# Optimization experiments

Hardware: AMD Instinct MI355X
Metric: run time of the kernel (lower is better)

## Reference

```python
import jax, jax.numpy as jnp
import numpy as np

D_MODEL = 1024
N_HEADS = 16
D_K = 64
BATCH = 2
SEQ = 2048
LN_EPS = 1e-5


def setup_inputs() -> dict:
    key = jax.random.key(0)
    ks = jax.random.split(key, 6)
    s = 1.0 / np.sqrt(D_MODEL)
    return {
        "h": jax.random.normal(ks[0], (BATCH, SEQ, D_MODEL), dtype=jnp.float32),
        "Wq": jax.random.normal(ks[1], (D_MODEL, D_MODEL), dtype=jnp.float32) * s,
        "bq": jnp.zeros((D_MODEL,), jnp.float32),
        "Wk": jax.random.normal(ks[2], (D_MODEL, D_MODEL), dtype=jnp.float32) * s,
        "bk": jnp.zeros((D_MODEL,), jnp.float32),
        "Wv": jax.random.normal(ks[3], (D_MODEL, D_MODEL), dtype=jnp.float32) * s,
        "bv": jnp.zeros((D_MODEL,), jnp.float32),
        "Wo": jax.random.normal(ks[4], (D_MODEL, D_MODEL), dtype=jnp.float32) * s,
        "bo": jnp.zeros((D_MODEL,), jnp.float32),
        "ln_w": jnp.ones((D_MODEL,), jnp.float32),
        "ln_b": jnp.zeros((D_MODEL,), jnp.float32),
    }


def _layernorm(x, w, b):
    mu = jnp.mean(x, axis=-1, keepdims=True)
    var = jnp.var(x, axis=-1, keepdims=True)
    return (x - mu) * jax.lax.rsqrt(var + LN_EPS) * w + b


def reference(h, Wq, bq, Wk, bk, Wv, bv, Wo, bo, ln_w, ln_b):
    b, s, _ = h.shape
    scale = 1.0 / np.sqrt(D_K)
    h_res = h
    hn = _layernorm(h, ln_w, ln_b)
    # Linear layers (torch convention: y = x @ W.T + b), split into heads
    q = (hn @ Wq.T + bq).reshape(b, s, N_HEADS, D_K)
    k = (hn @ Wk.T + bk).reshape(b, s, N_HEADS, D_K)
    v = (hn @ Wv.T + bv).reshape(b, s, N_HEADS, D_K)
    attn = jnp.einsum('bihd,bjhd->bhij', q, k) * scale  # [b, h, i, j]
    attn = jax.nn.softmax(attn, axis=-1)
    o = jnp.einsum('bhij,bjhd->bihd', attn, v).reshape(b, s, N_HEADS * D_K)
    out = o @ Wo.T + bo
    return out + h_res
```

## Files before the change

### kernel.cpp

```cpp
#include <hip/hip_runtime.h>
#include <cstdint>

#define D_MODEL 1024
#define N_HEADS 16
#define D_K     64
#define BATCH   2
#define SEQ     2048
#define TOKENS  (BATCH * SEQ)
#define LN_EPS  1e-5f
#define QSCALE  0.18033688011112042f

typedef __bf16 bf16x8 __attribute__((ext_vector_type(8)));
typedef float  floatx4 __attribute__((ext_vector_type(4)));

__device__ __forceinline__ unsigned short f2bf(float f) {
  union { float f; unsigned u; } v; v.f = f;
  unsigned r = v.u + 0x7fffu + ((v.u >> 16) & 1u);
  return (unsigned short)(r >> 16);
}
__device__ __forceinline__ unsigned short f2bf_fast(float f) {
  union { float f; unsigned u; } v; v.f = f;
  return (unsigned short)((v.u + 0x8000u) >> 16);
}

__device__ __forceinline__ void cp16(void* lds, const void* g) {
  __builtin_amdgcn_global_load_lds(
      (__attribute__((address_space(1))) void*)g,
      (__attribute__((address_space(3))) void*)lds, 16, 0, 0);
}

__global__ __launch_bounds__(256) void convw_kernel(
    const float* __restrict__ s0, const float* __restrict__ s1,
    const float* __restrict__ s2, const float* __restrict__ s3,
    unsigned short* __restrict__ dst) {
  int wsel = blockIdx.x >> 10;
  const float* s = (wsel == 0) ? s0 : (wsel == 1) ? s1 : (wsel == 2) ? s2 : s3;
  unsigned short* d = dst + ((size_t)wsel << 20);
  int i = ((blockIdx.x & 1023) << 8) + threadIdx.x;
  float4 v = reinterpret_cast<const float4*>(s)[i];
  ushort4 o;
  o.x = f2bf(v.x); o.y = f2bf(v.y); o.z = f2bf(v.z); o.w = f2bf(v.w);
  reinterpret_cast<ushort4*>(d)[i] = o;
}

__global__ __launch_bounds__(256) void ln_kernel(
    const float* __restrict__ h, const float* __restrict__ w,
    const float* __restrict__ b, unsigned short* __restrict__ hn) {
  int row = blockIdx.x;
  const float* x = h + (size_t)row * D_MODEL;
  float4 v = reinterpret_cast<const float4*>(x)[threadIdx.x];
  float s  = v.x + v.y + v.z + v.w;
  float s2 = v.x * v.x + v.y * v.y + v.z * v.z + v.w * v.w;
  for (int m = 1; m < 64; m <<= 1) {
    s  += __shfl_xor(s, m);
    s2 += __shfl_xor(s2, m);
  }
  __shared__ float ls[4], ls2[4];
  int wave = threadIdx.x >> 6;
  if ((threadIdx.x & 63) == 0) { ls[wave] = s; ls2[wave] = s2; }
  __syncthreads();
  s  = ls[0] + ls[1] + ls[2] + ls[3];
  s2 = ls2[0] + ls2[1] + ls2[2] + ls2[3];
  float mu  = s * (1.0f / D_MODEL);
  float var = s2 * (1.0f / D_MODEL) - mu * mu;
  float rs  = rsqrtf(var + LN_EPS);
  float4 wv = reinterpret_cast<const float4*>(w)[threadIdx.x];
  float4 bv = reinterpret_cast<const float4*>(b)[threadIdx.x];
  ushort4 o;
  o.x = f2bf((v.x - mu) * rs * wv.x + bv.x);
  o.y = f2bf((v.y - mu) * rs * wv.y + bv.y);
  o.z = f2bf((v.z - mu) * rs * wv.z + bv.z);
  o.w = f2bf((v.w - mu) * rs * wv.w + bv.w);
  reinterpret_cast<ushort4*>(hn + (size_t)row * D_MODEL)[threadIdx.x] = o;
}

__global__ __launch_bounds__(256) void gemm_qkv_kernel(
    const unsigned short* __restrict__ A, const unsigned short* __restrict__ Wcat,
    const float* __restrict__ bq, const float* __restrict__ bk,
    const float* __restrict__ bv,
    unsigned short* __restrict__ QK, unsigned short* __restrict__ VtG) {
  __shared__ unsigned short As[128 * 64];
  __shared__ unsigned short Bs[128 * 64];

  const int tid  = threadIdx.x;
  const int w    = tid >> 6;
  const int lane = tid & 63;
  const int l15  = lane & 15;
  const int quad = lane >> 4;
  const int sw   = l15 & 7;
  const int wm = (w >> 1) * 64;
  const int wn = (w & 1) * 64;
  const int bm = blockIdx.y * 128;
  const int bn = blockIdx.x * 128;

  const int srow = tid >> 3;
  const int swzc = (((tid & 7) ^ (srow & 7)) * 8);
  const unsigned short* ga = A    + (size_t)(bm + srow) * 1024 + swzc;
  const unsigned short* gb = Wcat + (size_t)(bn + srow) * 1024 + swzc;
  unsigned short* asl = As + w * 512;
  unsigned short* bsl = Bs + w * 512;

  floatx4 acc[4][4];
  for (int i = 0; i < 4; ++i)
    for (int j = 0; j < 4; ++j) acc[i][j] = {0.f, 0.f, 0.f, 0.f};

  for (int k0 = 0; k0 < 1024; k0 += 64) {
#pragma unroll
    for (int i = 0; i < 4; ++i) cp16(asl + i * 2048, ga + (size_t)i * 32 * 1024 + k0);
#pragma unroll
    for (int i = 0; i < 4; ++i) cp16(bsl + i * 2048, gb + (size_t)i * 32 * 1024 + k0);
    __syncthreads();
#pragma unroll
    for (int kb = 0; kb < 2; ++kb) {
      bf16x8 af[4], bfr[4];
#pragma unroll
      for (int mi = 0; mi < 4; ++mi)
        af[mi] = *reinterpret_cast<const bf16x8*>(
            As + (wm + mi * 16 + l15) * 64 + (((kb * 4 + quad) ^ sw) * 8));
#pragma unroll
      for (int ni = 0; ni < 4; ++ni)
        bfr[ni] = *reinterpret_cast<const bf16x8*>(
            Bs + (wn + ni * 16 + l15) * 64 + (((kb * 4 + quad) ^ sw) * 8));
#pragma unroll
      for (int mi = 0; mi < 4; ++mi)
#pragma unroll
        for (int ni = 0; ni < 4; ++ni)
          acc[mi][ni] = __builtin_amdgcn_mfma_f32_16x16x32_bf16(af[mi], bfr[ni], acc[mi][ni], 0, 0, 0);
    }
    __syncthreads();
  }

  const int wsel = blockIdx.x >> 3;
  if (wsel == 0) {
#pragma unroll
    for (int mi = 0; mi < 4; ++mi)
#pragma unroll
      for (int ni = 0; ni < 4; ++ni) {
        int col = bn + wn + ni * 16 + l15;
        float bb = bq[col];
#pragma unroll
        for (int r = 0; r < 4; ++r) {
          int row = bm + wm + mi * 16 + quad * 4 + r;
          QK[(size_t)row * 2048 + col] = f2bf((acc[mi][ni][r] + bb) * QSCALE);
        }
      }
  } else if (wsel == 1) {
#pragma unroll
    for (int mi = 0; mi < 4; ++mi)
#pragma unroll
      for (int ni = 0; ni < 4; ++ni) {
        int col = bn + wn + ni * 16 + l15;
        float bb = bk[col - 1024];
#pragma unroll
        for (int r = 0; r < 4; ++r) {
          int row = bm + wm + mi * 16 + quad * 4 + r;
          QK[(size_t)row * 2048 + col] = f2bf(acc[mi][ni][r] + bb);
        }
      }
  } else {
#pragma unroll
    for (int mi = 0; mi < 4; ++mi)
#pragma unroll
      for (int ni = 0; ni < 4; ++ni) {
        int d = bn + wn + ni * 16 + l15 - 2048;
        float bb = bv[d];
        ushort4 o;
        o.x = f2bf(acc[mi][ni][0] + bb);
        o.y = f2bf(acc[mi][ni][1] + bb);
        o.z = f2bf(acc[mi][ni][2] + bb);
        o.w = f2bf(acc[mi][ni][3] + bb);
        int row0 = bm + wm + mi * 16 + quad * 4;
        *reinterpret_cast<ushort4*>(VtG + (size_t)d * 4096 + row0) = o;
      }
  }
}

__global__ __launch_bounds__(256) void gemm_out_kernel(
    const unsigned short* __restrict__ A, const unsigned short* __restrict__ Bt,
    const float* __restrict__ bo, const float* __restrict__ resid,
    float* __restrict__ out) {
  __shared__ unsigned short As[128 * 64];
  __shared__ unsigned short Bs[64 * 64];

  const int tid  = threadIdx.x;
  const int w    = tid >> 6;
  const int lane = tid & 63;
  const int l15  = lane & 15;
  const int quad = lane >> 4;
  const int sw   = l15 & 7;
  const int wm = (w >> 1) * 64;
  const int wn = (w & 1) * 32;
  const int bm = blockIdx.y * 128;
  const int bn = blockIdx.x * 64;

  const int srow = tid >> 3;
  const int swzc = (((tid & 7) ^ (srow & 7)) * 8);
  const unsigned short* ga = A  + (size_t)(bm + srow) * 1024 + swzc;
  const unsigned short* gb = Bt + (size_t)(bn + srow) * 1024 + swzc;
  unsigned short* asl = As + w * 512;
  unsigned short* bsl = Bs + w * 512;

  floatx4 acc[4][2];
  for (int i = 0; i < 4; ++i)
    for (int j = 0; j < 2; ++j) acc[i][j] = {0.f, 0.f, 0.f, 0.f};

  for (int k0 = 0; k0 < 1024; k0 += 64) {
#pragma unroll
    for (int i = 0; i < 4; ++i) cp16(asl + i * 2048, ga + (size_t)i * 32 * 1024 + k0);
#pragma unroll
    for (int i = 0; i < 2; ++i) cp16(bsl + i * 2048, gb + (size_t)i * 32 * 1024 + k0);
    __syncthreads();
#pragma unroll
    for (int kb = 0; kb < 2; ++kb) {
      bf16x8 af[4], bfr[2];
#pragma unroll
      for (int mi = 0; mi < 4; ++mi)
        af[mi] = *reinterpret_cast<const bf16x8*>(
            As + (wm + mi * 16 + l15) * 64 + (((kb * 4 + quad) ^ sw) * 8));
#pragma unroll
      for (int ni = 0; ni < 2; ++ni)
        bfr[ni] = *reinterpret_cast<const bf16x8*>(
            Bs + (wn + ni * 16 + l15) * 64 + (((kb * 4 + quad) ^ sw) * 8));
#pragma unroll
      for (int mi = 0; mi < 4; ++mi)
#pragma unroll
        for (int ni = 0; ni < 2; ++ni)
          acc[mi][ni] = __builtin_amdgcn_mfma_f32_16x16x32_bf16(af[mi], bfr[ni], acc[mi][ni], 0, 0, 0);
    }
    __syncthreads();
  }

#pragma unroll
  for (int mi = 0; mi < 4; ++mi)
#pragma unroll
    for (int ni = 0; ni < 2; ++ni) {
      int col = bn + wn + ni * 16 + l15;
      float bb = bo[col];
#pragma unroll
      for (int r = 0; r < 4; ++r) {
        int row = bm + wm + mi * 16 + quad * 4 + r;
        size_t idx = (size_t)row * 1024 + col;
        out[idx] = acc[mi][ni][r] + bb + resid[idx];
      }
    }
}

__global__ __launch_bounds__(256) void attn_kernel(
    const unsigned short* __restrict__ QK, const unsigned short* __restrict__ VtG,
    unsigned short* __restrict__ O) {
  __shared__ unsigned short Ks[128 * 64];
  __shared__ unsigned short Vs[64 * 128];
  __shared__ unsigned short Pl[64 * 64];

  const int tid  = threadIdx.x;
  const int w    = tid >> 6;
  const int lane = tid & 63;
  const int l15  = lane & 15;
  const int quad = lane >> 4;
  const int sw   = l15 & 7;

  const int hh = blockIdx.x, qt = blockIdx.y, bz = blockIdx.z;
  const int tq0  = bz * SEQ + qt * 64;
  const int hoff = hh * 64;

  const unsigned short* qp = QK + (size_t)(tq0 + w * 16 + l15) * 2048 + hoff;
  bf16x8 qf0 = *reinterpret_cast<const bf16x8*>(qp + quad * 8);
  bf16x8 qf1 = *reinterpret_cast<const bf16x8*>(qp + 32 + quad * 8);

  bf16x8 ones;
#pragma unroll
  for (int j = 0; j < 8; ++j) ones[j] = (__bf16)1.0f;

  floatx4 oacc[4], lacc;
  for (int d = 0; d < 4; ++d) oacc[d] = {0.f, 0.f, 0.f, 0.f};
  lacc = {0.f, 0.f, 0.f, 0.f};

  const unsigned short* kg = QK + 1024 + hoff
      + (size_t)(bz * SEQ + (tid >> 3)) * 2048
      + (((tid & 7) ^ ((tid >> 3) & 7)) * 8);
  const unsigned short* vg = VtG
      + (size_t)(hoff + (tid >> 4)) * 4096 + bz * SEQ
      + (((tid & 15) ^ ((tid >> 4) & 7)) * 8);
  unsigned short* ksl = Ks + w * 512;
  unsigned short* vsl = Vs + w * 512;

  for (int kt = 0; kt < SEQ / 128; ++kt) {
    const unsigned short* kgi = kg + (size_t)(kt * 128) * 2048;
    const unsigned short* vgi = vg + kt * 128;
#pragma unroll
    for (int i = 0; i < 4; ++i) cp16(ksl + i * 2048, kgi + (size_t)(i * 32) * 2048);
#pragma unroll
    for (int i = 0; i < 4; ++i) cp16(vsl + i * 2048, vgi + (size_t)(i * 16) * 4096);
    __syncthreads();

    floatx4 sacc[8];
#pragma unroll
    for (int nb = 0; nb < 8; ++nb) sacc[nb] = {0.f, 0.f, 0.f, 0.f};
#pragma unroll
    for (int nb = 0; nb < 8; ++nb) {
      const unsigned short* krow = Ks + (nb * 16 + l15) * 64;
      bf16x8 b0 = *reinterpret_cast<const bf16x8*>(krow + ((quad ^ sw) * 8));
      bf16x8 b1 = *reinterpret_cast<const bf16x8*>(krow + (((4 + quad) ^ sw) * 8));
      sacc[nb] = __builtin_amdgcn_mfma_f32_16x16x32_bf16(qf0, b0, sacc[nb], 0, 0, 0);
      sacc[nb] = __builtin_amdgcn_mfma_f32_16x16x32_bf16(qf1, b1, sacc[nb], 0, 0, 0);
    }

#pragma unroll
    for (int nb = 0; nb < 8; ++nb)
#pragma unroll
      for (int r = 0; r < 4; ++r)
        sacc[nb][r] = __builtin_amdgcn_exp2f(sacc[nb][r]);

#pragma unroll
    for (int c = 0; c < 2; ++c) {
#pragma unroll
      for (int nb2 = 0; nb2 < 4; ++nb2) {
        int gc = 2 * nb2 + (l15 >> 3);
#pragma unroll
        for (int r = 0; r < 4; ++r) {
          int row = w * 16 + quad * 4 + r;
          Pl[row * 64 + ((gc ^ (row & 7)) * 8) + (l15 & 7)] =
              f2bf_fast(sacc[c * 4 + nb2][r]);
        }
      }
#pragma unroll
      for (int kb = 0; kb < 2; ++kb) {
        bf16x8 ap = *reinterpret_cast<const bf16x8*>(
            Pl + (w * 16 + l15) * 64 + (((kb * 4 + quad) ^ sw) * 8));
        lacc = __builtin_amdgcn_mfma_f32_16x16x32_bf16(ap, ones, lacc, 0, 0, 0);
#pragma unroll
        for (int d = 0; d < 4; ++d) {
          bf16x8 bvf = *reinterpret_cast<const bf16x8*>(
              Vs + (d * 16 + l15) * 128 + (((c * 8 + kb * 4 + quad) ^ sw) * 8));
          oacc[d] = __builtin_amdgcn_mfma_f32_16x16x32_bf16(ap, bvf, oacc[d], 0, 0, 0);
        }
      }
    }
    __syncthreads();
  }

#pragma unroll
  for (int r = 0; r < 4; ++r) {
    float inv = 1.0f / lacc[r];
    int row = w * 16 + quad * 4 + r;
#pragma unroll
    for (int d = 0; d < 4; ++d)
      Pl[row * 64 + d * 16 + l15] = f2bf_fast(oacc[d][r] * inv);
  }
  int orow = lane >> 2, ocol = (lane & 3) * 16;
  const unsigned short* prow = Pl + (w * 16 + orow) * 64 + ocol;
  uint4 ov0 = *reinterpret_cast<const uint4*>(prow);
  uint4 ov1 = *reinterpret_cast<const uint4*>(prow + 8);
  unsigned short* obase = O + (size_t)(tq0 + w * 16 + orow) * 1024 + hoff + ocol;
  *reinterpret_cast<uint4*>(obase)     = ov0;
  *reinterpret_cast<uint4*>(obase + 8) = ov1;
}

extern "C" void kernel_launch(void* const* d_in, const int* in_sizes, int n_in,
                              void* d_out, int out_size, void* d_ws, size_t ws_size,
                              hipStream_t stream) {
  const float* h    = (const float*)d_in[0];
  const float* Wq   = (const float*)d_in[1];
  const float* bq   = (const float*)d_in[2];
  const float* Wk   = (const float*)d_in[3];
  const float* bk   = (const float*)d_in[4];
  const float* Wv   = (const float*)d_in[5];
  const float* bv   = (const float*)d_in[6];
  const float* Wo   = (const float*)d_in[7];
  const float* bo   = (const float*)d_in[8];
  const float* ln_w = (const float*)d_in[9];
  const float* ln_b = (const float*)d_in[10];
  float* out = (float*)d_out;

  unsigned short* ws = (unsigned short*)d_ws;
  const size_t WSZ = (size_t)1 << 20;
  unsigned short* Wcat = ws;
  unsigned short* hn   = Wcat + 4 * WSZ;
  unsigned short* QKb  = hn + (size_t)TOKENS * D_MODEL;
  unsigned short* VtG  = QKb + (size_t)TOKENS * 2048;
  unsigned short* Obuf = VtG + (size_t)D_MODEL * TOKENS;

  convw_kernel<<<4096, 256, 0, stream>>>(Wq, Wk, Wv, Wo, Wcat);
  ln_kernel<<<TOKENS, 256, 0, stream>>>(h, ln_w, ln_b, hn);

  gemm_qkv_kernel<<<dim3(24, 32), 256, 0, stream>>>(hn, Wcat, bq, bk, bv, QKb, VtG);

  attn_kernel<<<dim3(N_HEADS, SEQ / 64, BATCH), 256, 0, stream>>>(QKb, VtG, Obuf);

  gemm_out_kernel<<<dim3(16, 32), 256, 0, stream>>>(Obuf, Wcat + 3 * WSZ, bo, h, out);
}
```

Before: 219.0 us.

## Double query rows per attention block and merge weight-convert with layernorm kernel

The attention kernel now handles 128 query rows per block, 32 per wave in two 16-row subtiles. Each K and V fragment loaded from LDS is reused across both subtiles, and S is computed transposed (K as A operand) so P can be written as packed ushort4 into a per-wave XOR-swizzled LDS region. The output is now written straight to global memory. The weight-conversion and layernorm kernels are merged into one launch to save a kernel launch. The attention grid halves, so there are fewer blocks and more registers per thread, which may reduce occupancy.

```diff
diff --git a/kernel.cpp b/kernel.cpp
--- a/kernel.cpp
+++ b/kernel.cpp
@@ -29,24 +29,24 @@
       (__attribute__((address_space(3))) void*)lds, 16, 0, 0);
 }
 
-__global__ __launch_bounds__(256) void convw_kernel(
-    const float* __restrict__ s0, const float* __restrict__ s1,
-    const float* __restrict__ s2, const float* __restrict__ s3,
-    unsigned short* __restrict__ dst) {
-  int wsel = blockIdx.x >> 10;
-  const float* s = (wsel == 0) ? s0 : (wsel == 1) ? s1 : (wsel == 2) ? s2 : s3;
-  unsigned short* d = dst + ((size_t)wsel << 20);
-  int i = ((blockIdx.x & 1023) << 8) + threadIdx.x;
-  float4 v = reinterpret_cast<const float4*>(s)[i];
-  ushort4 o;
-  o.x = f2bf(v.x); o.y = f2bf(v.y); o.z = f2bf(v.z); o.w = f2bf(v.w);
-  reinterpret_cast<ushort4*>(d)[i] = o;
-}
-
-__global__ __launch_bounds__(256) void ln_kernel(
-    const float* __restrict__ h, const float* __restrict__ w,
-    const float* __restrict__ b, unsigned short* __restrict__ hn) {
-  int row = blockIdx.x;
+__global__ __launch_bounds__(256) void prep_kernel(
+    const float* __restrict__ h, const float* __restrict__ w0,
+    const float* __restrict__ w1, const float* __restrict__ w2,
+    const float* __restrict__ w3, const float* __restrict__ lw,
+    const float* __restrict__ lb, unsigned short* __restrict__ Wcat,
+    unsigned short* __restrict__ hn) {
+  if (blockIdx.x < 4096) {
+    int wsel = blockIdx.x >> 10;
+    const float* s = (wsel == 0) ? w0 : (wsel == 1) ? w1 : (wsel == 2) ? w2 : w3;
+    unsigned short* d = Wcat + ((size_t)wsel << 20);
+    int i = ((blockIdx.x & 1023) << 8) + threadIdx.x;
+    float4 v = reinterpret_cast<const float4*>(s)[i];
+    ushort4 o;
+    o.x = f2bf(v.x); o.y = f2bf(v.y); o.z = f2bf(v.z); o.w = f2bf(v.w);
+    reinterpret_cast<ushort4*>(d)[i] = o;
+    return;
+  }
+  int row = blockIdx.x - 4096;
   const float* x = h + (size_t)row * D_MODEL;
   float4 v = reinterpret_cast<const float4*>(x)[threadIdx.x];
   float s  = v.x + v.y + v.z + v.w;
@@ -64,8 +64,8 @@
   float mu  = s * (1.0f / D_MODEL);
   float var = s2 * (1.0f / D_MODEL) - mu * mu;
   float rs  = rsqrtf(var + LN_EPS);
-  float4 wv = reinterpret_cast<const float4*>(w)[threadIdx.x];
-  float4 bv = reinterpret_cast<const float4*>(b)[threadIdx.x];
+  float4 wv = reinterpret_cast<const float4*>(lw)[threadIdx.x];
+  float4 bv = reinterpret_cast<const float4*>(lb)[threadIdx.x];
   ushort4 o;
   o.x = f2bf((v.x - mu) * rs * wv.x + bv.x);
   o.y = f2bf((v.y - mu) * rs * wv.y + bv.y);
@@ -250,7 +250,7 @@
     unsigned short* __restrict__ O) {
   __shared__ unsigned short Ks[128 * 64];
   __shared__ unsigned short Vs[64 * 128];
-  __shared__ unsigned short Pl[64 * 64];
+  __shared__ unsigned short Pl[4 * 32 * 128];
 
   const int tid  = threadIdx.x;
   const int w    = tid >> 6;
@@ -260,20 +260,29 @@
   const int sw   = l15 & 7;
 
   const int hh = blockIdx.x, qt = blockIdx.y, bz = blockIdx.z;
-  const int tq0  = bz * SEQ + qt * 64;
+  const int tq0  = bz * SEQ + qt * 128;
   const int hoff = hh * 64;
 
-  const unsigned short* qp = QK + (size_t)(tq0 + w * 16 + l15) * 2048 + hoff;
-  bf16x8 qf0 = *reinterpret_cast<const bf16x8*>(qp + quad * 8);
-  bf16x8 qf1 = *reinterpret_cast<const bf16x8*>(qp + 32 + quad * 8);
+  bf16x8 qf[2][2];
+#pragma unroll
+  for (int ms = 0; ms < 2; ++ms) {
+    const unsigned short* qp =
+        QK + (size_t)(tq0 + w * 32 + ms * 16 + l15) * 2048 + hoff;
+    qf[ms][0] = *reinterpret_cast<const bf16x8*>(qp + quad * 8);
+    qf[ms][1] = *reinterpret_cast<const bf16x8*>(qp + 32 + quad * 8);
+  }
 
   bf16x8 ones;
 #pragma unroll
   for (int j = 0; j < 8; ++j) ones[j] = (__bf16)1.0f;
 
-  floatx4 oacc[4], lacc;
-  for (int d = 0; d < 4; ++d) oacc[d] = {0.f, 0.f, 0.f, 0.f};
-  lacc = {0.f, 0.f, 0.f, 0.f};
+  floatx4 oacc[2][4], lacc[2];
+#pragma unroll
+  for (int ms = 0; ms < 2; ++ms) {
+    lacc[ms] = {0.f, 0.f, 0.f, 0.f};
+#pragma unroll
+    for (int d = 0; d < 4; ++d) oacc[ms][d] = {0.f, 0.f, 0.f, 0.f};
+  }
 
   const unsigned short* kg = QK + 1024 + hoff
       + (size_t)(bz * SEQ + (tid >> 3)) * 2048
@@ -283,6 +292,7 @@
       + (((tid & 15) ^ ((tid >> 4) & 7)) * 8);
   unsigned short* ksl = Ks + w * 512;
   unsigned short* vsl = Vs + w * 512;
+  unsigned short* wp  = Pl + w * 4096;
 
   for (int kt = 0; kt < SEQ / 128; ++kt) {
     const unsigned short* kgi = kg + (size_t)(kt * 128) * 2048;
@@ -293,67 +303,74 @@
     for (int i = 0; i < 4; ++i) cp16(vsl + i * 2048, vgi + (size_t)(i * 16) * 4096);
     __syncthreads();
 
-    floatx4 sacc[8];
-#pragma unroll
-    for (int nb = 0; nb < 8; ++nb) sacc[nb] = {0.f, 0.f, 0.f, 0.f};
+    floatx4 ss[2][8];
+#pragma unroll
+    for (int ms = 0; ms < 2; ++ms)
+#pragma unroll
+      for (int nb = 0; nb < 8; ++nb) ss[ms][nb] = {0.f, 0.f, 0.f, 0.f};
 #pragma unroll
     for (int nb = 0; nb < 8; ++nb) {
       const unsigned short* krow = Ks + (nb * 16 + l15) * 64;
-      bf16x8 b0 = *reinterpret_cast<const bf16x8*>(krow + ((quad ^ sw) * 8));
-      bf16x8 b1 = *reinterpret_cast<const bf16x8*>(krow + (((4 + quad) ^ sw) * 8));
-      sacc[nb] = __builtin_amdgcn_mfma_f32_16x16x32_bf16(qf0, b0, sacc[nb], 0, 0, 0);
-      sacc[nb] = __builtin_amdgcn_mfma_f32_16x16x32_bf16(qf1, b1, sacc[nb], 0, 0, 0);
-    }
-
-#pragma unroll
-    for (int nb = 0; nb < 8; ++nb)
-#pragma unroll
-      for (int r = 0; r < 4; ++r)
-        sacc[nb][r] = __builtin_amdgcn_exp2f(sacc[nb][r]);
-
-#pragma unroll
-    for (int c = 0; c < 2; ++c) {
-#pragma unroll
-      for (int nb2 = 0; nb2 < 4; ++nb2) {
-        int gc = 2 * nb2 + (l15 >> 3);
-#pragma unroll
-        for (int r = 0; r < 4; ++r) {
-          int row = w * 16 + quad * 4 + r;
-          Pl[row * 64 + ((gc ^ (row & 7)) * 8) + (l15 & 7)] =
-              f2bf_fast(sacc[c * 4 + nb2][r]);
-        }
-      }
-#pragma unroll
-      for (int kb = 0; kb < 2; ++kb) {
-        bf16x8 ap = *reinterpret_cast<const bf16x8*>(
-            Pl + (w * 16 + l15) * 64 + (((kb * 4 + quad) ^ sw) * 8));
-        lacc = __builtin_amdgcn_mfma_f32_16x16x32_bf16(ap, ones, lacc, 0, 0, 0);
-#pragma unroll
-        for (int d = 0; d < 4; ++d) {
-          bf16x8 bvf = *reinterpret_cast<const bf16x8*>(
-              Vs + (d * 16 + l15) * 128 + (((c * 8 + kb * 4 + quad) ^ sw) * 8));
-          oacc[d] = __builtin_amdgcn_mfma_f32_16x16x32_bf16(ap, bvf, oacc[d], 0, 0, 0);
-        }
-      }
-    }
-    __syncthreads();
-  }
-
-#pragma unroll
-  for (int r = 0; r < 4; ++r) {
-    float inv = 1.0f / lacc[r];
-    int row = w * 16 + quad * 4 + r;
-#pragma unroll
-    for (int d = 0; d < 4; ++d)
-      Pl[row * 64 + d * 16 + l15] = f2bf_fast(oacc[d][r] * inv);
-  }
-  int orow = lane >> 2, ocol = (lane & 3) * 16;
-  const unsigned short* prow = Pl + (w * 16 + orow) * 64 + ocol;
-  uint4 ov0 = *reinterpret_cast<const uint4*>(prow);
-  uint4 ov1 = *reinterpret_cast<const uint4*>(prow + 8);
-  unsigned short* obase = O + (size_t)(tq0 + w * 16 + orow) * 1024 + hoff + ocol;
-  *reinterpret_cast<uint4*>(obase)     = ov0;
-  *reinterpret_cast<uint4*>(obase + 8) = ov1;
+      bf16x8 kf0 = *reinterpret_cast<const bf16x8*>(krow + ((quad ^ sw) * 8));
+      bf16x8 kf1 = *reinterpret_cast<const bf16x8*>(krow + (((4 + quad) ^ sw) * 8));
+#pragma unroll
+      for (int ms = 0; ms < 2; ++ms) {
+        ss[ms][nb] = __builtin_amdgcn_mfma_f32_16x16x32_bf16(kf0, qf[ms][0], ss[ms][nb], 0, 0, 0);
+        ss[ms][nb] = __builtin_amdgcn_mfma_f32_16x16x32_bf16(kf1, qf[ms][1], ss[ms][nb], 0, 0, 0);
+      }
+    }
+
+#pragma unroll
+    for (int ms = 0; ms < 2; ++ms)
+#pragma unroll
+      for (int nb = 0; nb < 8; ++nb) {
+        ushort4 pk;
+        pk.x = f2bf_fast(__builtin_amdgcn_exp2f(ss[ms][nb][0]));
+        pk.y = f2bf_fast(__builtin_amdgcn_exp2f(ss[ms][nb][1]));
+        pk.z = f2bf_fast(__builtin_amdgcn_exp2f(ss[ms][nb][2]));
+        pk.w = f2bf_fast(__builtin_amdgcn_exp2f(ss[ms][nb][3]));
+        int rr = ms * 16 + l15;
+        int phys = (nb * 2 + (quad >> 1)) ^ l15;
+        *reinterpret_cast<ushort4*>(wp + rr * 128 + phys * 8 + (quad & 1) * 4) = pk;
+      }
+
+#pragma unroll
+    for (int kf = 0; kf < 4; ++kf) {
+      bf16x8 pf[2];
+#pragma unroll
+      for (int ms = 0; ms < 2; ++ms) {
+        int rr = ms * 16 + l15;
+        int phys = (kf * 4 + quad) ^ l15;
+        pf[ms] = *reinterpret_cast<const bf16x8*>(wp + rr * 128 + phys * 8);
+        lacc[ms] = __builtin_amdgcn_mfma_f32_16x16x32_bf16(ones, pf[ms], lacc[ms], 0, 0, 0);
+      }
+#pragma unroll
+      for (int db = 0; db < 4; ++db) {
+        bf16x8 vf = *reinterpret_cast<const bf16x8*>(
+            Vs + (db * 16 + l15) * 128 + (((kf * 4 + quad) ^ sw) * 8));
+#pragma unroll
+        for (int ms = 0; ms < 2; ++ms)
+          oacc[ms][db] = __builtin_amdgcn_mfma_f32_16x16x32_bf16(vf, pf[ms], oacc[ms][db], 0, 0, 0);
+      }
+    }
+    __syncthreads();
+  }
+
+#pragma unroll
+  for (int ms = 0; ms < 2; ++ms) {
+    float inv = 1.0f / lacc[ms][0];
+    unsigned short* ob = O + (size_t)(tq0 + w * 32 + ms * 16 + l15) * 1024
+                       + hoff + quad * 4;
+#pragma unroll
+    for (int db = 0; db < 4; ++db) {
+      ushort4 ov;
+      ov.x = f2bf_fast(oacc[ms][db][0] * inv);
+      ov.y = f2bf_fast(oacc[ms][db][1] * inv);
+      ov.z = f2bf_fast(oacc[ms][db][2] * inv);
+      ov.w = f2bf_fast(oacc[ms][db][3] * inv);
+      *reinterpret_cast<ushort4*>(ob + db * 16) = ov;
+    }
+  }
 }
 
 extern "C" void kernel_launch(void* const* d_in, const int* in_sizes, int n_in,
@@ -380,12 +397,11 @@
   unsigned short* VtG  = QKb + (size_t)TOKENS * 2048;
   unsigned short* Obuf = VtG + (size_t)D_MODEL * TOKENS;
 
-  convw_kernel<<<4096, 256, 0, stream>>>(Wq, Wk, Wv, Wo, Wcat);
-  ln_kernel<<<TOKENS, 256, 0, stream>>>(h, ln_w, ln_b, hn);
+  prep_kernel<<<8192, 256, 0, stream>>>(h, Wq, Wk, Wv, Wo, ln_w, ln_b, Wcat, hn);
 
   gemm_qkv_kernel<<<dim3(24, 32), 256, 0, stream>>>(hn, Wcat, bq, bk, bv, QKb, VtG);
 
-  attn_kernel<<<dim3(N_HEADS, SEQ / 64, BATCH), 256, 0, stream>>>(QKb, VtG, Obuf);
+  attn_kernel<<<dim3(N_HEADS, SEQ / 128, BATCH), 256, 0, stream>>>(QKb, VtG, Obuf);
 
   gemm_out_kernel<<<dim3(16, 32), 256, 0, stream>>>(Obuf, Wcat + 3 * WSZ, bo, h, out);
 }
```

New measurement: 206.7 us. -5.6%, faster.
